# Performance work log

Measured on AMD Instinct MI355X. Metric: run time of the kernel, lower is better.

## Reference

```python
import jax, jax.numpy as jnp
import numpy as np

B, S, H = 32, 512, 768
NHEAD, DH = 8, 96          # 8 heads * 96 = 768
E = 4096                   # edges per sample
NC = 2
NEG = -1e9
EPS = 1e-5


def _p(k, shape, scale=0.02):
    return scale * jax.random.normal(k, shape, dtype=jnp.float32)


def setup_inputs() -> dict:
    key = jax.random.key(0)
    ks = jax.random.split(key, 24)
    z = lambda *s: jnp.zeros(s, jnp.float32)
    return {
        "diff_encoded": jax.random.normal(ks[0], (B, S, H), jnp.float32),
        "msg_encoded": jax.random.normal(ks[1], (B, S, H), jnp.float32),
        "msg_mask": jnp.ones((B, S), jnp.int32),
        "edge_index_diff": jax.random.randint(ks[2], (B, 2, E), 0, S),
        "edge_index_msg": jax.random.randint(ks[3], (B, 2, E), 0, S),
        # GATv2Conv(heads=1): lin_l (source/message), lin_r (target), att vector, output bias
        "gat_wl": _p(ks[4], (H, H)), "gat_bl": z(H),
        "gat_wr": _p(ks[5], (H, H)), "gat_br": z(H),
        "gat_att": _p(ks[6], (H,)), "gat_bias": z(H),
        # cross MultiheadAttention
        "wq": _p(ks[7], (H, H)), "bq": z(H),
        "wk": _p(ks[8], (H, H)), "bk": z(H),
        "wv": _p(ks[9], (H, H)), "bv": z(H),
        "wo": _p(ks[10], (H, H)), "bo": z(H),
        # LayerNorm + MLP head
        "ln_g": jnp.ones((H,), jnp.float32), "ln_b": z(H),
        "fc0_w": _p(ks[11], (H, 512)), "fc0_b": z(512),
        "fc1_w": _p(ks[12], (512, 128)), "fc1_b": z(128),
        "fc2_w": _p(ks[13], (128, NC)), "fc2_b": z(NC),
    }


def _gat_single(x, edges, wl, bl, wr, br, att, bias):
    # GATv2Conv, heads=1, add_self_loops=True. x: [N,H], edges: [2,E] (src, dst).
    N = x.shape[0]
    src, dst = edges[0], edges[1]
    valid = (src < N) & (dst < N)            # clip_edge_index, as a mask
    src = jnp.where(valid, src, 0)
    dst = jnp.where(valid, dst, 0)
    loop = jnp.arange(N, dtype=src.dtype)    # PyG adds self loops
    src_a = jnp.concatenate([src, loop])
    dst_a = jnp.concatenate([dst, loop])
    valid_a = jnp.concatenate([valid, jnp.ones((N,), bool)])
    xl = x @ wl + bl                          # source / message transform
    xr = x @ wr + br                          # target transform
    e = jax.nn.leaky_relu(xl[src_a] + xr[dst_a], 0.2) @ att   # [E+N]
    e = jnp.where(valid_a, e, NEG)
    emax = jax.ops.segment_max(e, dst_a, num_segments=N)
    p = jnp.exp(e - emax[dst_a]) * valid_a.astype(x.dtype)
    denom = jax.ops.segment_sum(p, dst_a, num_segments=N)
    alpha = p / denom[dst_a]
    out = jax.ops.segment_sum(alpha[:, None] * xl[src_a], dst_a, num_segments=N)
    return out + bias


_gat = jax.vmap(_gat_single, in_axes=(0, 0) + (None,) * 6)


def _layernorm(x, g, b):
    mu = jnp.mean(x, -1, keepdims=True)
    var = jnp.mean(jnp.square(x - mu), -1, keepdims=True)
    return (x - mu) * jax.lax.rsqrt(var + EPS) * g + b


def reference(diff_encoded, msg_encoded, msg_mask, edge_index_diff, edge_index_msg,
              gat_wl, gat_bl, gat_wr, gat_br, gat_att, gat_bias,
              wq, bq, wk, bk, wv, bv, wo, bo, ln_g, ln_b,
              fc0_w, fc0_b, fc1_w, fc1_b, fc2_w, fc2_b):
    diff_g = _gat(diff_encoded, edge_index_diff, gat_wl, gat_bl, gat_wr, gat_br, gat_att, gat_bias) + diff_encoded
    msg_g = _gat(msg_encoded, edge_index_msg, gat_wl, gat_bl, gat_wr, gat_br, gat_att, gat_bias) + msg_encoded
    # cross attention: query=diff_g, key/value=msg_g, key_padding_mask = (msg_mask == 0)
    q = (diff_g @ wq + bq).reshape(B, S, NHEAD, DH)
    k = (msg_g @ wk + bk).reshape(B, S, NHEAD, DH)
    v = (msg_g @ wv + bv).reshape(B, S, NHEAD, DH)
    scores = jnp.einsum("bqhd,bkhd->bhqk", q, k) / jnp.sqrt(jnp.float32(DH))
    scores = jnp.where((msg_mask == 0)[:, None, None, :], NEG, scores)
    attn = jax.nn.softmax(scores, axis=-1)
    ctx = jnp.einsum("bhqk,bkhd->bqhd", attn, v).reshape(B, S, H) @ wo + bo
    fused = _layernorm(ctx + diff_g, ln_g, ln_b)
    x = fused[:, 0, :]                                  # CLS token
    x = jax.nn.relu(x @ fc0_w + fc0_b)                  # dropout = identity (eval)
    x = jax.nn.relu(x @ fc1_w + fc1_b)
    return x @ fc2_w + fc2_b
```

## Files before the change

### kernel.cpp

```cpp
#include <hip/hip_runtime.h>
#include <hip/hip_bf16.h>
#include <math.h>

#define BB 32
#define SS 512
#define HH 768
#define NHEADC 8
#define DHC 96
#define EE 4096
#define NCC 2
#define CAPC 128
#define CAP2 32
#define GSL 36
#define NEGV -1000000000.0f
#define EPSV 1e-5f

#define PREP_CVT  12288
#define PREP_WT   2304
#define PREP_BIAS 3
#define PREP_CNT  512
#define PREP_TOT  (PREP_CVT + PREP_WT + PREP_BIAS + PREP_CNT)

typedef __hip_bfloat16 bf16;
typedef __bf16 bf16x8 __attribute__((ext_vector_type(8)));
typedef float f32x4 __attribute__((ext_vector_type(4)));

static __device__ inline unsigned short f2bf_u(float f) {
  __hip_bfloat16 h = __float2bfloat16(f);
  return *(unsigned short*)&h;
}
static __device__ inline float bfu(unsigned short u) {
  return __uint_as_float(((unsigned int)u) << 16);
}
static __device__ inline float bf2f(bf16 h) { return __bfloat162float(h); }

static __device__ inline void gload16(const void* g, void* l) {
  __builtin_amdgcn_global_load_lds(
      (const __attribute__((address_space(1))) void*)g,
      (__attribute__((address_space(3))) void*)l, 16, 0, 0);
}

__global__ __launch_bounds__(256) void k_prep(
    const float* __restrict__ msg_enc, bf16* __restrict__ Abf,
    const float* __restrict__ gat_wl, const float* __restrict__ gat_wr,
    const float* __restrict__ wk, const float* __restrict__ wv,
    bf16* __restrict__ wtA, bf16* __restrict__ wtB,
    const float* __restrict__ gat_bl, const float* __restrict__ gat_br,
    const float* __restrict__ bk, const float* __restrict__ bv,
    float* __restrict__ biasA, float* __restrict__ biasB,
    const int* __restrict__ e_diff,
    int* __restrict__ dcnt, int* __restrict__ dsrc)
{
  int blk = blockIdx.x, tid = threadIdx.x;
  if (blk < PREP_CVT) {
    int i = (blk * 256 + tid) * 4;
    float4 v = *(const float4*)(msg_enc + i);
    ushort4 o;
    o.x = f2bf_u(v.x); o.y = f2bf_u(v.y); o.z = f2bf_u(v.z); o.w = f2bf_u(v.w);
    *(ushort4*)((unsigned short*)Abf + i) = o;
    return;
  }
  blk -= PREP_CVT;
  if (blk < PREP_WT) {
    int z = blk / 576, rr = blk - z * 576;
    int bx = rr % 24, by = rr / 24;
    const float* w; bf16* o;
    switch (z) {
      case 0: w = gat_wl; o = wtA; break;
      case 1: w = gat_wr; o = wtA + (size_t)HH * HH; break;
      case 2: w = wk;     o = wtB; break;
      default: w = wv;    o = wtB + (size_t)HH * HH; break;
    }
    __shared__ float t[32][33];
    int n0 = bx * 32, k0 = by * 32;
    int x = tid & 31, y = tid >> 5;
    for (int yy = y; yy < 32; yy += 8)
      t[yy][x] = w[(size_t)(k0 + yy) * HH + n0 + x];
    __syncthreads();
    for (int yy = y; yy < 32; yy += 8)
      o[(size_t)(n0 + yy) * HH + k0 + x] = __float2bfloat16(t[x][yy]);
    return;
  }
  blk -= PREP_WT;
  if (blk < PREP_BIAS) {
    int t = blk * 256 + tid;
    if (t < HH) {
      biasA[t] = gat_bl[t]; biasA[HH + t] = gat_br[t];
      biasB[t] = bk[t];     biasB[HH + t] = bv[t];
    }
    return;
  }
  blk -= PREP_BIAS;
  {
    int i = blk * 256 + tid;
    if (i >= BB * EE) return;
    int b = i / EE, j = i - b * EE;
    int s2 = e_diff[b * 2 * EE + j], d2 = e_diff[b * 2 * EE + EE + j];
    if (s2 >= 0 && s2 < SS && d2 == 0) {
      int pos = atomicAdd(&dcnt[b], 1);
      if (pos < CAPC) dsrc[b * CAPC + pos] = s2;
    }
    if (j == 0) {
      int pos = atomicAdd(&dcnt[b], 1);
      if (pos < CAPC) dsrc[b * CAPC + pos] = 0;
    }
  }
}

__global__ __launch_bounds__(512) void k_bin(
    const int* __restrict__ e_msg, int* __restrict__ cnt,
    int* __restrict__ offs, int* __restrict__ binned)
{
  __shared__ int lc[SS];
  __shared__ int tmp[SS];
  int b = blockIdx.x, t = threadIdx.x;
  lc[t] = 0;
  __syncthreads();
  int ss[8], dd[8];
  #pragma unroll
  for (int r = 0; r < 8; ++r) {
    int j = r * 512 + t;
    ss[r] = e_msg[b * 2 * EE + j];
    dd[r] = e_msg[b * 2 * EE + EE + j];
    if (ss[r] >= 0 && ss[r] < SS && dd[r] >= 0 && dd[r] < SS)
      atomicAdd(&lc[dd[r]], 1);
    else
      dd[r] = -1;
  }
  __syncthreads();
  int x = lc[t];
  tmp[t] = x;
  __syncthreads();
  for (int off = 1; off < SS; off <<= 1) {
    int u = (t >= off) ? tmp[t - off] : 0;
    __syncthreads();
    tmp[t] += u;
    __syncthreads();
  }
  int ex = tmp[t] - x;
  cnt[b * SS + t] = x;
  offs[b * SS + t] = ex;
  __syncthreads();
  lc[t] = ex;
  __syncthreads();
  #pragma unroll
  for (int r = 0; r < 8; ++r) {
    if (dd[r] >= 0) {
      int pos = atomicAdd(&lc[dd[r]], 1);
      binned[(size_t)b * EE + pos] = ss[r];
    }
  }
}

template <typename OT>
__global__ __launch_bounds__(256) void k_gemm(
    const bf16* __restrict__ A, const bf16* __restrict__ Bt,
    const float* __restrict__ bias, OT* __restrict__ C0, OT* __restrict__ C1,
    int M, int K)
{
  __shared__ __align__(16) bf16 As0[128 * 32];
  __shared__ __align__(16) bf16 As1[128 * 32];
  __shared__ __align__(16) bf16 Bs0[128 * 32];
  __shared__ __align__(16) bf16 Bs1[128 * 32];
  const int tid = threadIdx.x;
  const int wv = tid >> 6, lane = tid & 63;
  const int bm = blockIdx.x * 128, bn = blockIdx.y * 128;
  const int wm = (wv & 1) * 64, wn = (wv >> 1) * 64;
  const int m16 = lane & 15, half = lane >> 4;
  f32x4 acc[4][4];
  #pragma unroll
  for (int i = 0; i < 4; ++i)
    #pragma unroll
    for (int j = 0; j < 4; ++j) acc[i][j] = (f32x4){0.f, 0.f, 0.f, 0.f};

  const int c0 = tid, c1 = tid + 256;
  const int r0 = c0 >> 2, o0 = (c0 & 3) * 8;
  const int r1 = c1 >> 2, o1 = (c1 & 3) * 8;
  const size_t aB0 = (size_t)(bm + r0) * K + o0;
  const size_t aB1 = (size_t)(bm + r1) * K + o1;
  const size_t bB0 = (size_t)(bn + r0) * K + o0;
  const size_t bB1 = (size_t)(bn + r1) * K + o1;

  for (int k0 = 0; k0 < K; k0 += 64) {
    __syncthreads();
    gload16(A + aB0 + k0, As0 + (size_t)c0 * 8);
    gload16(A + aB1 + k0, As0 + (size_t)c1 * 8);
    gload16(A + aB0 + k0 + 32, As1 + (size_t)c0 * 8);
    gload16(A + aB1 + k0 + 32, As1 + (size_t)c1 * 8);
    gload16(Bt + bB0 + k0, Bs0 + (size_t)c0 * 8);
    gload16(Bt + bB1 + k0, Bs0 + (size_t)c1 * 8);
    gload16(Bt + bB0 + k0 + 32, Bs1 + (size_t)c0 * 8);
    gload16(Bt + bB1 + k0 + 32, Bs1 + (size_t)c1 * 8);
    __syncthreads();
    #pragma unroll
    for (int ks = 0; ks < 2; ++ks) {
      const bf16* Ah = ks ? As1 : As0;
      const bf16* Bh = ks ? Bs1 : Bs0;
      bf16x8 af[4], bfv[4];
      #pragma unroll
      for (int t = 0; t < 4; ++t) {
        af[t]  = *(const bf16x8*)(Ah + (wm + t * 16 + m16) * 32 + half * 8);
        bfv[t] = *(const bf16x8*)(Bh + (wn + t * 16 + m16) * 32 + half * 8);
      }
      #pragma unroll
      for (int i = 0; i < 4; ++i)
        #pragma unroll
        for (int j = 0; j < 4; ++j)
          acc[i][j] = __builtin_amdgcn_mfma_f32_16x16x32_bf16(af[i], bfv[j], acc[i][j], 0, 0, 0);
    }
  }
  #pragma unroll
  for (int i = 0; i < 4; ++i) {
    #pragma unroll
    for (int j = 0; j < 4; ++j) {
      int col = bn + wn + j * 16 + m16;
      float bv = bias ? bias[col] : 0.f;
      OT* Cb = (col < HH) ? C0 : C1;
      int cc = (col < HH) ? col : col - HH;
      #pragma unroll
      for (int r = 0; r < 4; ++r) {
        int row = bm + wm + i * 16 + half * 4 + r;
        float v = acc[i][j][r] + bv;
        if constexpr (sizeof(OT) == 2)
          Cb[(size_t)row * HH + cc] = (OT)__float2bfloat16(v);
        else
          Cb[(size_t)row * HH + cc] = v;
      }
    }
  }
}

__global__ __launch_bounds__(512) void k_gemm256(
    const bf16* __restrict__ A, const bf16* __restrict__ Bt,
    const float* __restrict__ bias, bf16* __restrict__ C0, bf16* __restrict__ C1)
{
  constexpr int K = 768;
  constexpr int NT = K / 64;
  __shared__ __align__(16) bf16 Asm[3][256 * 64];
  __shared__ __align__(16) bf16 Bsm[3][128 * 64];

  const int tid = threadIdx.x;
  const int wv = tid >> 6, lane = tid & 63;
  const int m16 = lane & 15, half = lane >> 4;

  const int bid = blockIdx.x;
  const int swz = (bid & 7) * 96 + (bid >> 3);
  const int bm = (swz / 12) * 256;
  const int bn = (swz % 12) * 128;

  const int wm = (wv >> 1) * 64;
  const int wn = (wv & 1) * 64;

  size_t srcA[4], srcB[2];
  #pragma unroll
  for (int li = 0; li < 4; ++li) {
    int L = li * 512 + tid;
    int row = L >> 3;
    int g = (L & 7) ^ (row & 7);
    srcA[li] = (size_t)(bm + row) * K + g * 8;
  }
  #pragma unroll
  for (int li = 0; li < 2; ++li) {
    int L = li * 512 + tid;
    int row = L >> 3;
    int g = (L & 7) ^ (row & 7);
    srcB[li] = (size_t)(bn + row) * K + g * 8;
  }

  auto stage = [&](int t, bf16* ba, bf16* bb) {
    #pragma unroll
    for (int li = 0; li < 4; ++li)
      gload16(A + srcA[li] + (size_t)t * 64, ba + (size_t)(li * 512 + tid) * 8);
    #pragma unroll
    for (int li = 0; li < 2; ++li)
      gload16(Bt + srcB[li] + (size_t)t * 64, bb + (size_t)(li * 512 + tid) * 8);
  };

  f32x4 acc[4][4];
  #pragma unroll
  for (int i = 0; i < 4; ++i)
    #pragma unroll
    for (int j = 0; j < 4; ++j) acc[i][j] = (f32x4){0.f, 0.f, 0.f, 0.f};

  const int xr = m16 & 7;
  const int aoff0 = (wm + m16) * 64 + ((half ^ xr) * 8);
  const int aoff1 = (wm + m16) * 64 + (((4 + half) ^ xr) * 8);
  const int boff0 = (wn + m16) * 64 + ((half ^ xr) * 8);
  const int boff1 = (wn + m16) * 64 + (((4 + half) ^ xr) * 8);

  auto tile = [&](const bf16* __restrict__ Ab, const bf16* __restrict__ Bb) {
    bf16x8 b0[4], b1[4], a0[2], a1[2], a2[2], a3[2];
    #pragma unroll
    for (int j = 0; j < 4; ++j) b0[j] = *(const bf16x8*)(Bb + boff0 + j * 1024);
    #pragma unroll
    for (int i = 0; i < 2; ++i) a0[i] = *(const bf16x8*)(Ab + aoff0 + i * 1024);
    __builtin_amdgcn_s_setprio(1);
    #pragma unroll
    for (int i = 0; i < 2; ++i)
      #pragma unroll
      for (int j = 0; j < 4; ++j)
        acc[i][j] = __builtin_amdgcn_mfma_f32_16x16x32_bf16(a0[i], b0[j], acc[i][j], 0, 0, 0);
    __builtin_amdgcn_s_setprio(0);
    #pragma unroll
    for (int i = 0; i < 2; ++i) a1[i] = *(const bf16x8*)(Ab + aoff0 + (i + 2) * 1024);
    __builtin_amdgcn_s_setprio(1);
    #pragma unroll
    for (int i = 0; i < 2; ++i)
      #pragma unroll
      for (int j = 0; j < 4; ++j)
        acc[i + 2][j] = __builtin_amdgcn_mfma_f32_16x16x32_bf16(a1[i], b0[j], acc[i + 2][j], 0, 0, 0);
    __builtin_amdgcn_s_setprio(0);
    #pragma unroll
    for (int j = 0; j < 4; ++j) b1[j] = *(const bf16x8*)(Bb + boff1 + j * 1024);
    #pragma unroll
    for (int i = 0; i < 2; ++i) a2[i] = *(const bf16x8*)(Ab + aoff1 + i * 1024);
    __builtin_amdgcn_s_setprio(1);
    #pragma unroll
    for (int i = 0; i < 2; ++i)
      #pragma unroll
      for (int j = 0; j < 4; ++j)
        acc[i][j] = __builtin_amdgcn_mfma_f32_16x16x32_bf16(a2[i], b1[j], acc[i][j], 0, 0, 0);
    __builtin_amdgcn_s_setprio(0);
    #pragma unroll
    for (int i = 0; i < 2; ++i) a3[i] = *(const bf16x8*)(Ab + aoff1 + (i + 2) * 1024);
    __builtin_amdgcn_s_setprio(1);
    #pragma unroll
    for (int i = 0; i < 2; ++i)
      #pragma unroll
      for (int j = 0; j < 4; ++j)
        acc[i + 2][j] = __builtin_amdgcn_mfma_f32_16x16x32_bf16(a3[i], b1[j], acc[i + 2][j], 0, 0, 0);
    __builtin_amdgcn_s_setprio(0);
  };

  auto step = [&](int kt, int cur, int nxt) {
    if (kt == NT - 1) asm volatile("s_waitcnt vmcnt(0)" ::: "memory");
    else              asm volatile("s_waitcnt vmcnt(6)" ::: "memory");
    __builtin_amdgcn_s_barrier();
    __builtin_amdgcn_sched_barrier(0);
    if (kt + 2 < NT) stage(kt + 2, Asm[nxt], Bsm[nxt]);
    tile(Asm[cur], Bsm[cur]);
  };

  stage(0, Asm[0], Bsm[0]);
  stage(1, Asm[1], Bsm[1]);
  for (int kt3 = 0; kt3 < NT; kt3 += 3) {
    step(kt3 + 0, 0, 2);
    step(kt3 + 1, 1, 0);
    step(kt3 + 2, 2, 1);
  }

  #pragma unroll
  for (int i = 0; i < 4; ++i) {
    #pragma unroll
    for (int j = 0; j < 4; ++j) {
      int col = bn + wn + j * 16 + m16;
      float bv = bias[col];
      bf16* Cb = (col < HH) ? C0 : C1;
      int cc = (col < HH) ? col : col - HH;
      #pragma unroll
      for (int r = 0; r < 4; ++r) {
        int row = bm + wm + i * 16 + half * 4 + r;
        Cb[(size_t)row * HH + cc] = (bf16)__float2bfloat16(acc[i][j][r] + bv);
      }
    }
  }
}

__global__ __launch_bounds__(256) void k_gat_fused(
    const int* __restrict__ binned, const int* __restrict__ offs,
    const int* __restrict__ cnt, const bf16* __restrict__ xl,
    const bf16* __restrict__ xrb, const float* __restrict__ att,
    const float* __restrict__ gbias, const bf16* __restrict__ resid,
    bf16* __restrict__ out)
{
  int bid = blockIdx.x;
  int xcd = bid & 7, idx = bid >> 3;
  int b = xcd * 4 + (idx >> 7);
  int d = (idx & 127) * 4 + (threadIdx.x >> 6);
  int lane = threadIdx.x & 63;
  int base = offs[b * SS + d], n = cnt[b * SS + d];
  const int* bin = binned + (size_t)b * EE + base;
  float av[12];
  {
    const float4* a4 = (const float4*)att;
    #pragma unroll
    for (int r = 0; r < 3; ++r) {
      float4 t = a4[lane + 64 * r];
      av[4*r] = t.x; av[4*r+1] = t.y; av[4*r+2] = t.z; av[4*r+3] = t.w;
    }
  }
  float xr[12];
  {
    const ushort4* p = (const ushort4*)(xrb + ((size_t)b * SS + d) * HH);
    #pragma unroll
    for (int r = 0; r < 3; ++r) {
      ushort4 v = p[lane + 64 * r];
      xr[4*r] = bfu(v.x); xr[4*r+1] = bfu(v.y); xr[4*r+2] = bfu(v.z); xr[4*r+3] = bfu(v.w);
    }
  }
  float m = -3.0e38f, l = 0.f;
  float acc[12] = {};
  int nn = n + 1;
  ushort4 pre[3];
  {
    const ushort4* p = (const ushort4*)(xl + ((size_t)b * SS + d) * HH);
    pre[0] = p[lane]; pre[1] = p[lane + 64]; pre[2] = p[lane + 128];
  }
  for (int j = 0; j < nn; ++j) {
    ushort4 cur0 = pre[0], cur1 = pre[1], cur2 = pre[2];
    if (j + 1 < nn) {
      int sn = bin[j];
      const ushort4* p = (const ushort4*)(xl + ((size_t)b * SS + sn) * HH);
      pre[0] = p[lane]; pre[1] = p[lane + 64]; pre[2] = p[lane + 128];
    }
    float xs[12];
    xs[0] = bfu(cur0.x); xs[1] = bfu(cur0.y); xs[2]  = bfu(cur0.z); xs[3]  = bfu(cur0.w);
    xs[4] = bfu(cur1.x); xs[5] = bfu(cur1.y); xs[6]  = bfu(cur1.z); xs[7]  = bfu(cur1.w);
    xs[8] = bfu(cur2.x); xs[9] = bfu(cur2.y); xs[10] = bfu(cur2.z); xs[11] = bfu(cur2.w);
    float e = 0.f;
    #pragma unroll
    for (int k = 0; k < 12; ++k) {
      float t = xs[k] + xr[k];
      t = t > 0.f ? t : 0.2f * t;
      e += t * av[k];
    }
    #pragma unroll
    for (int off = 32; off > 0; off >>= 1) e += __shfl_xor(e, off);
    float mn = fmaxf(m, e);
    float so = __expf(m - mn);
    float w  = __expf(e - mn);
    l = l * so + w;
    #pragma unroll
    for (int k = 0; k < 12; ++k) acc[k] = acc[k] * so + w * xs[k];
    m = mn;
  }
  float inv = 1.f / l;
  size_t o = ((size_t)b * SS + d) * HH;
  const float4* gb4 = (const float4*)gbias;
  const ushort4* rs4 = (const ushort4*)(resid + o);
  ushort4* out4 = (ushort4*)(out + o);
  #pragma unroll
  for (int r = 0; r < 3; ++r) {
    int c = lane + 64 * r;
    float4 gg = gb4[c];
    ushort4 rr = rs4[c];
    ushort4 ov;
    ov.x = f2bf_u(acc[4*r+0] * inv + gg.x + bfu(rr.x));
    ov.y = f2bf_u(acc[4*r+1] * inv + gg.y + bfu(rr.y));
    ov.z = f2bf_u(acc[4*r+2] * inv + gg.z + bfu(rr.z));
    ov.w = f2bf_u(acc[4*r+3] * inv + gg.w + bfu(rr.w));
    out4[c] = ov;
  }
}

__global__ __launch_bounds__(192) void k_gather_diff(
    const int* __restrict__ dcnt, const int* __restrict__ dsrc,
    const float* __restrict__ diff_enc, bf16* __restrict__ G)
{
  int b = blockIdx.y, jj = blockIdx.x;
  int n = min(dcnt[b], CAP2);
  int t = threadIdx.x;
  size_t orow = ((size_t)b * GSL + jj) * HH;
  ushort4 o = {0, 0, 0, 0};
  if (jj < n || jj == CAP2) {
    int s = (jj == CAP2) ? 0 : dsrc[b * CAPC + jj];
    float4 v = ((const float4*)(diff_enc + ((size_t)b * SS + s) * HH))[t];
    o.x = f2bf_u(v.x); o.y = f2bf_u(v.y); o.z = f2bf_u(v.z); o.w = f2bf_u(v.w);
  }
  *(ushort4*)((unsigned short*)G + orow + t * 4) = o;
}

__global__ __launch_bounds__(256) void k_diff_gat0(
    const int* __restrict__ dcnt, const float* __restrict__ GDl,
    const float* __restrict__ GDr, const float* __restrict__ att,
    const float* __restrict__ gbias, const float* __restrict__ diff_enc,
    float* __restrict__ dg0)
{
  int b = blockIdx.x;
  int n = min(dcnt[b], CAP2);
  __shared__ float ee[CAP2];
  __shared__ float al[CAP2];
  __shared__ float xr0s[HH];
  int wave = threadIdx.x >> 6, lane = threadIdx.x & 63;
  for (int h = threadIdx.x; h < HH; h += 256)
    xr0s[h] = GDr[((size_t)b * GSL + CAP2) * HH + h];
  __syncthreads();
  for (int jj = wave; jj < n; jj += 4) {
    const float* px = GDl + ((size_t)b * GSL + jj) * HH;
    float part = 0.f;
    #pragma unroll
    for (int r = 0; r < HH / 64; ++r) {
      int h = lane + 64 * r;
      float t = px[h] + xr0s[h];
      t = t > 0.f ? t : 0.2f * t;
      part += t * att[h];
    }
    #pragma unroll
    for (int off = 32; off > 0; off >>= 1) part += __shfl_xor(part, off);
    if (lane == 0) ee[jj] = part;
  }
  __syncthreads();
  if (threadIdx.x == 0) {
    float m = -3.0e38f;
    for (int i = 0; i < n; ++i) m = fmaxf(m, ee[i]);
    float ssum = 0.f;
    for (int i = 0; i < n; ++i) ssum += expf(ee[i] - m);
    float inv = 1.f / ssum;
    for (int i = 0; i < n; ++i) al[i] = expf(ee[i] - m) * inv;
  }
  __syncthreads();
  for (int h = threadIdx.x; h < HH; h += 256) {
    float acc = 0.f;
    for (int i = 0; i < n; ++i) acc += al[i] * GDl[((size_t)b * GSL + i) * HH + h];
    dg0[b * HH + h] = acc + gbias[h] + diff_enc[(size_t)b * SS * HH + h];
  }
}

__global__ __launch_bounds__(256) void k_colmat(
    const float* __restrict__ in, const float* __restrict__ w,
    const float* __restrict__ bias, const float* __restrict__ extra,
    float* __restrict__ outp, int Kd, int Nd, long in_stride, int relu)
{
  int b = blockIdx.y, n0 = blockIdx.x * 64;
  int tid = threadIdx.x, wv = tid >> 6, lane = tid & 63;
  __shared__ float xs[HH];
  __shared__ float red[4][64];
  const float* src = in + (size_t)b * in_stride;
  for (int k = tid; k < Kd; k += 256) xs[k] = src[k];
  __syncthreads();
  int h = n0 + lane;
  int kpw = Kd >> 2;
  int kb = wv * kpw;
  float acc = 0.f;
  for (int k = 0; k < kpw; k += 8) {
    #pragma unroll
    for (int u = 0; u < 8; ++u) {
      int kk = kb + k + u;
      acc += xs[kk] * w[(size_t)kk * Nd + h];
    }
  }
  red[wv][lane] = acc;
  __syncthreads();
  if (tid < 64) {
    float s = red[0][tid] + red[1][tid] + red[2][tid] + red[3][tid] + bias[n0 + tid];
    if (extra) s += extra[(size_t)b * Nd + n0 + tid];
    if (relu) s = fmaxf(s, 0.f);
    outp[(size_t)b * Nd + n0 + tid] = s;
  }
}

__global__ __launch_bounds__(256) void k_lnfc0(
    const float* __restrict__ fpre, const float* __restrict__ g,
    const float* __restrict__ bta,
    const float* __restrict__ fc0w, const float* __restrict__ fc0b,
    float* __restrict__ a0g)
{
  int b = blockIdx.y, n0 = blockIdx.x * 64;
  int tid = threadIdx.x, wv = tid >> 6, lane = tid & 63;
  __shared__ float xs[HH];
  __shared__ float red[4][64];
  __shared__ float rs[4], rq[4];
  float v0 = fpre[b * HH + tid];
  float v1 = fpre[b * HH + tid + 256];
  float v2 = fpre[b * HH + tid + 512];
  float sum = v0 + v1 + v2;
  float sq = v0 * v0 + v1 * v1 + v2 * v2;
  #pragma unroll
  for (int off = 32; off > 0; off >>= 1) { sum += __shfl_xor(sum, off); sq += __shfl_xor(sq, off); }
  if (lane == 0) { rs[wv] = sum; rq[wv] = sq; }
  __syncthreads();
  sum = rs[0] + rs[1] + rs[2] + rs[3];
  sq = rq[0] + rq[1] + rq[2] + rq[3];
  float mu = sum / HH;
  float var = sq / HH - mu * mu;
  float scl = rsqrtf(var + EPSV);
  xs[tid]       = (v0 - mu) * scl * g[tid]       + bta[tid];
  xs[tid + 256] = (v1 - mu) * scl * g[tid + 256] + bta[tid + 256];
  xs[tid + 512] = (v2 - mu) * scl * g[tid + 512] + bta[tid + 512];
  __syncthreads();
  int h = n0 + lane;
  int kb = wv * 192;
  float acc = 0.f;
  for (int k = 0; k < 192; k += 8) {
    #pragma unroll
    for (int u = 0; u < 8; ++u) {
      int kk = kb + k + u;
      acc += xs[kk] * fc0w[(size_t)kk * 512 + h];
    }
  }
  red[wv][lane] = acc;
  __syncthreads();
  if (tid < 64) {
    float s = red[0][tid] + red[1][tid] + red[2][tid] + red[3][tid] + fc0b[n0 + tid];
    a0g[(size_t)b * 512 + n0 + tid] = fmaxf(s, 0.f);
  }
}

__global__ __launch_bounds__(256) void k_fc12(
    const float* __restrict__ a0g, const float* __restrict__ fc1w,
    const float* __restrict__ fc1b, const float* __restrict__ fc2w,
    const float* __restrict__ fc2b, float* __restrict__ out)
{
  int b = blockIdx.x, tid = threadIdx.x;
  __shared__ float a0s[512];
  __shared__ float a1s[128];
  __shared__ float r1[2][128];
  for (int k = tid; k < 512; k += 256) a0s[k] = a0g[b * 512 + k];
  __syncthreads();
  int o = tid & 127, hf = tid >> 7;
  int kb = hf * 256;
  float acc = 0.f;
  for (int k = 0; k < 256; k += 8) {
    #pragma unroll
    for (int u = 0; u < 8; ++u) {
      int kk = kb + k + u;
      acc += a0s[kk] * fc1w[(size_t)kk * 128 + o];
    }
  }
  r1[hf][o] = acc;
  __syncthreads();
  if (tid < 128) a1s[tid] = fmaxf(r1[0][tid] + r1[1][tid] + fc1b[tid], 0.f);
  __syncthreads();
  if (tid < 128) {
    int oo = tid >> 6, l = tid & 63;
    float p = a1s[l] * fc2w[l * 2 + oo] + a1s[l + 64] * fc2w[(l + 64) * 2 + oo];
    #pragma unroll
    for (int off = 32; off > 0; off >>= 1) p += __shfl_xor(p, off);
    if (l == 0) out[b * NCC + oo] = p + fc2b[oo];
  }
}

__global__ __launch_bounds__(512) void k_attn(
    const float* __restrict__ dg0, const float* __restrict__ wq,
    const float* __restrict__ bq, const bf16* __restrict__ kb,
    const bf16* __restrict__ vb, const int* __restrict__ mask,
    float* __restrict__ ctx)
{
  int b = blockIdx.x / NHEADC, hd = blockIdx.x % NHEADC;
  __shared__ float xg[HH];
  __shared__ float qs[DHC];
  __shared__ float sc[SS];
  __shared__ float redm[8];
  __shared__ float reds[8];
  __shared__ float pr4[4][DHC];
  int tid = threadIdx.x;
  for (int k = tid; k < HH; k += 512) xg[k] = dg0[b * HH + k];
  __syncthreads();
  if (tid < 384) {
    int d = tid >> 2, q = tid & 3;
    const float* wcol = wq + (size_t)(hd * DHC + d);
    float p = 0.f;
    int k0 = q * 192;
    for (int k = 0; k < 192; k += 8) {
      #pragma unroll
      for (int u = 0; u < 8; ++u)
        p += xg[k0 + k + u] * wcol[(size_t)(k0 + k + u) * HH];
    }
    p += __shfl_xor(p, 1);
    p += __shfl_xor(p, 2);
    if (q == 0) qs[d] = p + bq[hd * DHC + d];
  }
  __syncthreads();
  const float scale = 0.10206207261596575f;
  {
    int s = tid;
    const int4* pk4 = (const int4*)(kb + ((size_t)b * SS + s) * HH + hd * DHC);
    float acc = 0.f;
    #pragma unroll
    for (int c = 0; c < 12; ++c) {
      int4 raw = pk4[c];
      const unsigned short* u = (const unsigned short*)&raw;
      #pragma unroll
      for (int j = 0; j < 8; ++j) acc += qs[c * 8 + j] * bfu(u[j]);
    }
    sc[s] = (mask[b * SS + s] != 0) ? acc * scale : NEGV;
  }
  __syncthreads();
  int wave = tid >> 6, lane = tid & 63;
  float m = sc[tid];
  #pragma unroll
  for (int off = 32; off > 0; off >>= 1) m = fmaxf(m, __shfl_xor(m, off));
  if (lane == 0) redm[wave] = m;
  __syncthreads();
  m = redm[0];
  #pragma unroll
  for (int i = 1; i < 8; ++i) m = fmaxf(m, redm[i]);
  float p0 = expf(sc[tid] - m);
  float ssum = p0;
  #pragma unroll
  for (int off = 32; off > 0; off >>= 1) ssum += __shfl_xor(ssum, off);
  if (lane == 0) reds[wave] = ssum;
  __syncthreads();
  ssum = reds[0] + reds[1] + reds[2] + reds[3] + reds[4] + reds[5] + reds[6] + reds[7];
  float inv = 1.f / ssum;
  sc[tid] = p0 * inv;
  __syncthreads();
  {
    int hs = tid >> 7, d = tid & 127;
    if (d < DHC) {
      const bf16* pv = vb + ((size_t)b * SS + hs * 128) * HH + hd * DHC + d;
      float acc = 0.f;
      for (int s = 0; s < 128; s += 8) {
        #pragma unroll
        for (int u = 0; u < 8; ++u)
          acc += sc[hs * 128 + s + u] * bf2f(pv[(size_t)(s + u) * HH]);
      }
      pr4[hs][d] = acc;
    }
  }
  __syncthreads();
  if (tid < DHC)
    ctx[b * HH + hd * DHC + tid] = pr4[0][tid] + pr4[1][tid] + pr4[2][tid] + pr4[3][tid];
}

extern "C" void kernel_launch(void* const* d_in, const int* in_sizes, int n_in,
                              void* d_out, int out_size, void* d_ws, size_t ws_size,
                              hipStream_t stream) {
  const float* diff_enc = (const float*)d_in[0];
  const float* msg_enc  = (const float*)d_in[1];
  const int*   msg_mask = (const int*)d_in[2];
  const int*   e_diff   = (const int*)d_in[3];
  const int*   e_msg    = (const int*)d_in[4];
  const float* gat_wl   = (const float*)d_in[5];
  const float* gat_bl   = (const float*)d_in[6];
  const float* gat_wr   = (const float*)d_in[7];
  const float* gat_br   = (const float*)d_in[8];
  const float* gat_att  = (const float*)d_in[9];
  const float* gat_bias = (const float*)d_in[10];
  const float* wq = (const float*)d_in[11];
  const float* bq = (const float*)d_in[12];
  const float* wk = (const float*)d_in[13];
  const float* bk = (const float*)d_in[14];
  const float* wv = (const float*)d_in[15];
  const float* bv = (const float*)d_in[16];
  const float* wo = (const float*)d_in[17];
  const float* bo = (const float*)d_in[18];
  const float* ln_g = (const float*)d_in[19];
  const float* ln_b = (const float*)d_in[20];
  const float* fc0w = (const float*)d_in[21];
  const float* fc0b = (const float*)d_in[22];
  const float* fc1w = (const float*)d_in[23];
  const float* fc1b = (const float*)d_in[24];
  const float* fc2w = (const float*)d_in[25];
  const float* fc2b = (const float*)d_in[26];
  float* out = (float*)d_out;

  char* ws = (char*)d_ws;
  size_t off = 0;
  auto alloc = [&](size_t bytes) -> void* {
    void* p = (void*)(ws + off);
    off += (bytes + 255) & ~(size_t)255;
    return p;
  };
  bf16* Abf    = (bf16*)alloc((size_t)BB * SS * HH * 2);
  bf16* xl     = (bf16*)alloc((size_t)BB * SS * HH * 2);
  bf16* xrb    = (bf16*)alloc((size_t)BB * SS * HH * 2);
  bf16* kbuf   = (bf16*)alloc((size_t)BB * SS * HH * 2);
  bf16* vbuf   = (bf16*)alloc((size_t)BB * SS * HH * 2);
  bf16* mg     = (bf16*)alloc((size_t)BB * SS * HH * 2);
  bf16* wtA    = (bf16*)alloc((size_t)2 * HH * HH * 2);
  bf16* wtB    = (bf16*)alloc((size_t)2 * HH * HH * 2);
  float* biasA = (float*)alloc((size_t)2 * HH * 4);
  float* biasB = (float*)alloc((size_t)2 * HH * 4);
  int*   cnt   = (int*)alloc((size_t)BB * SS * 4);
  int*   offs  = (int*)alloc((size_t)BB * SS * 4);
  int*   binned= (int*)alloc((size_t)BB * EE * 4);
  bf16*  G     = (bf16*)alloc((size_t)BB * GSL * HH * 2);
  float* GDl   = (float*)alloc((size_t)BB * GSL * HH * 4);
  float* GDr   = (float*)alloc((size_t)BB * GSL * HH * 4);
  int*   dcnt  = (int*)alloc((size_t)BB * 4);
  int*   dsrc  = (int*)alloc((size_t)BB * CAPC * 4);
  float* dg0   = (float*)alloc((size_t)BB * HH * 4);
  float* ctx   = (float*)alloc((size_t)BB * HH * 4);
  float* fpre  = (float*)alloc((size_t)BB * HH * 4);
  float* a0g   = (float*)alloc((size_t)BB * 512 * 4);

  hipMemsetAsync(dcnt, 0, (size_t)BB * 4, stream);

  k_prep<<<PREP_TOT, 256, 0, stream>>>(msg_enc, Abf, gat_wl, gat_wr, wk, wv,
                                       wtA, wtB, gat_bl, gat_br, bk, bv,
                                       biasA, biasB, e_diff, dcnt, dsrc);
  k_bin<<<BB, 512, 0, stream>>>(e_msg, cnt, offs, binned);

  k_gemm256<<<768, 512, 0, stream>>>(Abf, wtA, biasA, xl, xrb);
  k_gat_fused<<<(BB * SS) / 4, 256, 0, stream>>>(binned, offs, cnt, xl, xrb,
                                                 gat_att, gat_bias, Abf, mg);
  k_gemm256<<<768, 512, 0, stream>>>(mg, wtB, biasB, kbuf, vbuf);
  {
    dim3 gBlk(256);
    dim3 gg(GSL, BB);
    k_gather_diff<<<gg, 192, 0, stream>>>(dcnt, dsrc, diff_enc, G);
    dim3 gGridD((BB * GSL) / 128, (2 * HH) / 128);
    k_gemm<float><<<gGridD, gBlk, 0, stream>>>(G, wtA, biasA, GDl, GDr, BB * GSL, HH);
  }
  k_diff_gat0<<<BB, 256, 0, stream>>>(dcnt, GDl, GDr, gat_att, gat_bias, diff_enc, dg0);
  k_attn<<<BB * NHEADC, 512, 0, stream>>>(dg0, wq, bq, kbuf, vbuf, msg_mask, ctx);
  {
    dim3 g(HH / 64, BB);
    k_colmat<<<g, 256, 0, stream>>>(ctx, wo, bo, dg0, fpre, HH, HH, HH, 0);
  }
  {
    dim3 g(512 / 64, BB);
    k_lnfc0<<<g, 256, 0, stream>>>(fpre, ln_g, ln_b, fc0w, fc0b, a0g);
  }
  k_fc12<<<BB, 256, 0, stream>>>(a0g, fc1w, fc1b, fc2w, fc2b, out);
}
```

Baseline: 424.6 us.

## Fold edge binning into prep and merge diff-gather GEMM into main GEMM

Merges the msg-edge binning kernel and the diff-edge collection into the prep kernel, with the diff collection now done through shared memory instead of global atomics. This removes the memset and a separate launch. The gathered diff rows (GSL raised to 40 so the row count divides into 256-row tiles) are appended after the msg activations, so one larger k_gemm256 launch computes both xl/xr and GDl/GDr. Its XCD swizzle is generalised to arbitrary tile counts. The intent is fewer launches and no small, poorly occupied separate GEMM, at the cost of slightly more padded rows and a heavier prep block.

```diff
diff --git a/kernel.cpp b/kernel.cpp
--- a/kernel.cpp
+++ b/kernel.cpp
@@ -11,15 +11,15 @@
 #define NCC 2
 #define CAPC 128
 #define CAP2 32
-#define GSL 36
+#define GSL 40
 #define NEGV -1000000000.0f
 #define EPSV 1e-5f
 
-#define PREP_CVT  12288
+#define PREP_CVT  6144
 #define PREP_WT   2304
-#define PREP_BIAS 3
-#define PREP_CNT  512
-#define PREP_TOT  (PREP_CVT + PREP_WT + PREP_BIAS + PREP_CNT)
+#define PREP_BIAS 2
+#define PREP_BIN  BB
+#define PREP_TOT  (PREP_CVT + PREP_WT + PREP_BIAS + PREP_BIN)
 
 typedef __hip_bfloat16 bf16;
 typedef __bf16 bf16x8 __attribute__((ext_vector_type(8)));
@@ -40,7 +40,7 @@
       (__attribute__((address_space(3))) void*)l, 16, 0, 0);
 }
 
-__global__ __launch_bounds__(256) void k_prep(
+__global__ __launch_bounds__(512) void k_prep(
     const float* __restrict__ msg_enc, bf16* __restrict__ Abf,
     const float* __restrict__ gat_wl, const float* __restrict__ gat_wr,
     const float* __restrict__ wk, const float* __restrict__ wv,
@@ -48,12 +48,13 @@
     const float* __restrict__ gat_bl, const float* __restrict__ gat_br,
     const float* __restrict__ bk, const float* __restrict__ bv,
     float* __restrict__ biasA, float* __restrict__ biasB,
-    const int* __restrict__ e_diff,
+    const int* __restrict__ e_msg, const int* __restrict__ e_diff,
+    int* __restrict__ cnt, int* __restrict__ offs, int* __restrict__ binned,
     int* __restrict__ dcnt, int* __restrict__ dsrc)
 {
   int blk = blockIdx.x, tid = threadIdx.x;
   if (blk < PREP_CVT) {
-    int i = (blk * 256 + tid) * 4;
+    int i = (blk * 512 + tid) * 4;
     float4 v = *(const float4*)(msg_enc + i);
     ushort4 o;
     o.x = f2bf_u(v.x); o.y = f2bf_u(v.y); o.z = f2bf_u(v.z); o.w = f2bf_u(v.w);
@@ -74,16 +75,16 @@
     __shared__ float t[32][33];
     int n0 = bx * 32, k0 = by * 32;
     int x = tid & 31, y = tid >> 5;
-    for (int yy = y; yy < 32; yy += 8)
+    for (int yy = y; yy < 32; yy += 16)
       t[yy][x] = w[(size_t)(k0 + yy) * HH + n0 + x];
     __syncthreads();
-    for (int yy = y; yy < 32; yy += 8)
+    for (int yy = y; yy < 32; yy += 16)
       o[(size_t)(n0 + yy) * HH + k0 + x] = __float2bfloat16(t[x][yy]);
     return;
   }
   blk -= PREP_WT;
   if (blk < PREP_BIAS) {
-    int t = blk * 256 + tid;
+    int t = blk * 512 + tid;
     if (t < HH) {
       biasA[t] = gat_bl[t]; biasA[HH + t] = gat_br[t];
       biasB[t] = bk[t];     biasB[HH + t] = bv[t];
@@ -92,139 +93,63 @@
   }
   blk -= PREP_BIAS;
   {
-    int i = blk * 256 + tid;
-    if (i >= BB * EE) return;
-    int b = i / EE, j = i - b * EE;
-    int s2 = e_diff[b * 2 * EE + j], d2 = e_diff[b * 2 * EE + EE + j];
-    if (s2 >= 0 && s2 < SS && d2 == 0) {
-      int pos = atomicAdd(&dcnt[b], 1);
-      if (pos < CAPC) dsrc[b * CAPC + pos] = s2;
-    }
-    if (j == 0) {
-      int pos = atomicAdd(&dcnt[b], 1);
-      if (pos < CAPC) dsrc[b * CAPC + pos] = 0;
-    }
-  }
-}
-
-__global__ __launch_bounds__(512) void k_bin(
-    const int* __restrict__ e_msg, int* __restrict__ cnt,
-    int* __restrict__ offs, int* __restrict__ binned)
-{
-  __shared__ int lc[SS];
-  __shared__ int tmp[SS];
-  int b = blockIdx.x, t = threadIdx.x;
-  lc[t] = 0;
-  __syncthreads();
-  int ss[8], dd[8];
-  #pragma unroll
-  for (int r = 0; r < 8; ++r) {
-    int j = r * 512 + t;
-    ss[r] = e_msg[b * 2 * EE + j];
-    dd[r] = e_msg[b * 2 * EE + EE + j];
-    if (ss[r] >= 0 && ss[r] < SS && dd[r] >= 0 && dd[r] < SS)
-      atomicAdd(&lc[dd[r]], 1);
-    else
-      dd[r] = -1;
-  }
-  __syncthreads();
-  int x = lc[t];
-  tmp[t] = x;
-  __syncthreads();
-  for (int off = 1; off < SS; off <<= 1) {
-    int u = (t >= off) ? tmp[t - off] : 0;
+    __shared__ int lc[SS];
+    __shared__ int tmp[SS];
+    __shared__ int dls[CAPC];
+    __shared__ int dn;
+    int b = blk, t = tid;
+    lc[t] = 0;
+    if (t == 0) dn = 0;
     __syncthreads();
-    tmp[t] += u;
+    int se[8], de[8];
+    #pragma unroll
+    for (int r = 0; r < 8; ++r) {
+      int j = r * 512 + t;
+      se[r] = e_msg[b * 2 * EE + j];
+      de[r] = e_msg[b * 2 * EE + EE + j];
+      if (se[r] >= 0 && se[r] < SS && de[r] >= 0 && de[r] < SS)
+        atomicAdd(&lc[de[r]], 1);
+      else
+        de[r] = -1;
+    }
+    #pragma unroll
+    for (int r = 0; r < 8; ++r) {
+      int j = r * 512 + t;
+      int s2 = e_diff[b * 2 * EE + j], d2 = e_diff[b * 2 * EE + EE + j];
+      if (s2 >= 0 && s2 < SS && d2 == 0) {
+        int p = atomicAdd(&dn, 1);
+        if (p < CAPC) dls[p] = s2;
+      }
+    }
+    if (t == 0) {
+      int p = atomicAdd(&dn, 1);
+      if (p < CAPC) dls[p] = 0;
+    }
     __syncthreads();
-  }
-  int ex = tmp[t] - x;
-  cnt[b * SS + t] = x;
-  offs[b * SS + t] = ex;
-  __syncthreads();
-  lc[t] = ex;
-  __syncthreads();
-  #pragma unroll
-  for (int r = 0; r < 8; ++r) {
-    if (dd[r] >= 0) {
-      int pos = atomicAdd(&lc[dd[r]], 1);
-      binned[(size_t)b * EE + pos] = ss[r];
-    }
-  }
-}
-
-template <typename OT>
-__global__ __launch_bounds__(256) void k_gemm(
-    const bf16* __restrict__ A, const bf16* __restrict__ Bt,
-    const float* __restrict__ bias, OT* __restrict__ C0, OT* __restrict__ C1,
-    int M, int K)
-{
-  __shared__ __align__(16) bf16 As0[128 * 32];
-  __shared__ __align__(16) bf16 As1[128 * 32];
-  __shared__ __align__(16) bf16 Bs0[128 * 32];
-  __shared__ __align__(16) bf16 Bs1[128 * 32];
-  const int tid = threadIdx.x;
-  const int wv = tid >> 6, lane = tid & 63;
-  const int bm = blockIdx.x * 128, bn = blockIdx.y * 128;
-  const int wm = (wv & 1) * 64, wn = (wv >> 1) * 64;
-  const int m16 = lane & 15, half = lane >> 4;
-  f32x4 acc[4][4];
-  #pragma unroll
-  for (int i = 0; i < 4; ++i)
-    #pragma unroll
-    for (int j = 0; j < 4; ++j) acc[i][j] = (f32x4){0.f, 0.f, 0.f, 0.f};
-
-  const int c0 = tid, c1 = tid + 256;
-  const int r0 = c0 >> 2, o0 = (c0 & 3) * 8;
-  const int r1 = c1 >> 2, o1 = (c1 & 3) * 8;
-  const size_t aB0 = (size_t)(bm + r0) * K + o0;
-  const size_t aB1 = (size_t)(bm + r1) * K + o1;
-  const size_t bB0 = (size_t)(bn + r0) * K + o0;
-  const size_t bB1 = (size_t)(bn + r1) * K + o1;
-
-  for (int k0 = 0; k0 < K; k0 += 64) {
+    int x = lc[t];
+    tmp[t] = x;
     __syncthreads();
-    gload16(A + aB0 + k0, As0 + (size_t)c0 * 8);
-    gload16(A + aB1 + k0, As0 + (size_t)c1 * 8);
-    gload16(A + aB0 + k0 + 32, As1 + (size_t)c0 * 8);
-    gload16(A + aB1 + k0 + 32, As1 + (size_t)c1 * 8);
-    gload16(Bt + bB0 + k0, Bs0 + (size_t)c0 * 8);
-    gload16(Bt + bB1 + k0, Bs0 + (size_t)c1 * 8);
-    gload16(Bt + bB0 + k0 + 32, Bs1 + (size_t)c0 * 8);
-    gload16(Bt + bB1 + k0 + 32, Bs1 + (size_t)c1 * 8);
+    for (int off = 1; off < SS; off <<= 1) {
+      int u = (t >= off) ? tmp[t - off] : 0;
+      __syncthreads();
+      tmp[t] += u;
+      __syncthreads();
+    }
+    int ex = tmp[t] - x;
+    cnt[b * SS + t] = x;
+    offs[b * SS + t] = ex;
+    int dnl = dn;
+    if (t == 0) dcnt[b] = dnl;
+    if (dnl > CAPC) dnl = CAPC;
+    for (int i2 = t; i2 < dnl; i2 += 512) dsrc[b * CAPC + i2] = dls[i2];
     __syncthreads();
-    #pragma unroll
-    for (int ks = 0; ks < 2; ++ks) {
-      const bf16* Ah = ks ? As1 : As0;
-      const bf16* Bh = ks ? Bs1 : Bs0;
-      bf16x8 af[4], bfv[4];
-      #pragma unroll
-      for (int t = 0; t < 4; ++t) {
-        af[t]  = *(const bf16x8*)(Ah + (wm + t * 16 + m16) * 32 + half * 8);
-        bfv[t] = *(const bf16x8*)(Bh + (wn + t * 16 + m16) * 32 + half * 8);
-      }
-      #pragma unroll
-      for (int i = 0; i < 4; ++i)
-        #pragma unroll
-        for (int j = 0; j < 4; ++j)
-          acc[i][j] = __builtin_amdgcn_mfma_f32_16x16x32_bf16(af[i], bfv[j], acc[i][j], 0, 0, 0);
-    }
-  }
-  #pragma unroll
-  for (int i = 0; i < 4; ++i) {
-    #pragma unroll
-    for (int j = 0; j < 4; ++j) {
-      int col = bn + wn + j * 16 + m16;
-      float bv = bias ? bias[col] : 0.f;
-      OT* Cb = (col < HH) ? C0 : C1;
-      int cc = (col < HH) ? col : col - HH;
-      #pragma unroll
-      for (int r = 0; r < 4; ++r) {
-        int row = bm + wm + i * 16 + half * 4 + r;
-        float v = acc[i][j][r] + bv;
-        if constexpr (sizeof(OT) == 2)
-          Cb[(size_t)row * HH + cc] = (OT)__float2bfloat16(v);
-        else
-          Cb[(size_t)row * HH + cc] = v;
+    lc[t] = ex;
+    __syncthreads();
+    #pragma unroll
+    for (int r = 0; r < 8; ++r) {
+      if (de[r] >= 0) {
+        int pos = atomicAdd(&lc[de[r]], 1);
+        binned[(size_t)b * EE + pos] = se[r];
       }
     }
   }
@@ -232,10 +157,13 @@
 
 __global__ __launch_bounds__(512) void k_gemm256(
     const bf16* __restrict__ A, const bf16* __restrict__ Bt,
-    const float* __restrict__ bias, bf16* __restrict__ C0, bf16* __restrict__ C1)
+    const float* __restrict__ bias,
+    bf16* __restrict__ C0, bf16* __restrict__ C1,
+    float* __restrict__ D0, float* __restrict__ D1, int nmt)
 {
   constexpr int K = 768;
   constexpr int NT = K / 64;
+  constexpr int M0 = BB * SS;
   __shared__ __align__(16) bf16 Asm[3][256 * 64];
   __shared__ __align__(16) bf16 Bsm[3][128 * 64];
 
@@ -244,7 +172,10 @@
   const int m16 = lane & 15, half = lane >> 4;
 
   const int bid = blockIdx.x;
-  const int swz = (bid & 7) * 96 + (bid >> 3);
+  const int nwg = nmt * 12;
+  const int qq = nwg >> 3, rm = nwg & 7;
+  const int xcd = bid & 7, iblk = bid >> 3;
+  const int swz = (xcd < rm ? xcd * (qq + 1) : rm * (qq + 1) + (xcd - rm) * qq) + iblk;
   const int bm = (swz / 12) * 256;
   const int bn = (swz % 12) * 128;
 
@@ -349,18 +280,28 @@
     step(kt3 + 2, 2, 1);
   }
 
+  const bool isD = (bm >= M0);
   #pragma unroll
   for (int i = 0; i < 4; ++i) {
     #pragma unroll
     for (int j = 0; j < 4; ++j) {
       int col = bn + wn + j * 16 + m16;
       float bv = bias[col];
-      bf16* Cb = (col < HH) ? C0 : C1;
       int cc = (col < HH) ? col : col - HH;
-      #pragma unroll
-      for (int r = 0; r < 4; ++r) {
-        int row = bm + wm + i * 16 + half * 4 + r;
-        Cb[(size_t)row * HH + cc] = (bf16)__float2bfloat16(acc[i][j][r] + bv);
+      if (!isD) {
+        bf16* Cb = (col < HH) ? C0 : C1;
+        #pragma unroll
+        for (int rj = 0; rj < 4; ++rj) {
+          int row = bm + wm + i * 16 + half * 4 + rj;
+          Cb[(size_t)row * HH + cc] = (bf16)__float2bfloat16(acc[i][j][rj] + bv);
+        }
+      } else {
+        float* Db = (col < HH) ? D0 : D1;
+        #pragma unroll
+        for (int rj = 0; rj < 4; ++rj) {
+          int row = bm + wm + i * 16 + half * 4 + rj - M0;
+          Db[(size_t)row * HH + cc] = acc[i][j][rj] + bv;
+        }
       }
     }
   }
@@ -752,7 +693,8 @@
     off += (bytes + 255) & ~(size_t)255;
     return p;
   };
-  bf16* Abf    = (bf16*)alloc((size_t)BB * SS * HH * 2);
+  bf16* Abf    = (bf16*)alloc((size_t)(BB * SS + BB * GSL) * HH * 2);
+  bf16* G      = Abf + (size_t)BB * SS * HH;
   bf16* xl     = (bf16*)alloc((size_t)BB * SS * HH * 2);
   bf16* xrb    = (bf16*)alloc((size_t)BB * SS * HH * 2);
   bf16* kbuf   = (bf16*)alloc((size_t)BB * SS * HH * 2);
@@ -765,7 +707,6 @@
   int*   cnt   = (int*)alloc((size_t)BB * SS * 4);
   int*   offs  = (int*)alloc((size_t)BB * SS * 4);
   int*   binned= (int*)alloc((size_t)BB * EE * 4);
-  bf16*  G     = (bf16*)alloc((size_t)BB * GSL * HH * 2);
   float* GDl   = (float*)alloc((size_t)BB * GSL * HH * 4);
   float* GDr   = (float*)alloc((size_t)BB * GSL * HH * 4);
   int*   dcnt  = (int*)alloc((size_t)BB * 4);
@@ -775,24 +716,19 @@
   float* fpre  = (float*)alloc((size_t)BB * HH * 4);
   float* a0g   = (float*)alloc((size_t)BB * 512 * 4);
 
-  hipMemsetAsync(dcnt, 0, (size_t)BB * 4, stream);
-
-  k_prep<<<PREP_TOT, 256, 0, stream>>>(msg_enc, Abf, gat_wl, gat_wr, wk, wv,
+  k_prep<<<PREP_TOT, 512, 0, stream>>>(msg_enc, Abf, gat_wl, gat_wr, wk, wv,
                                        wtA, wtB, gat_bl, gat_br, bk, bv,
-                                       biasA, biasB, e_diff, dcnt, dsrc);
-  k_bin<<<BB, 512, 0, stream>>>(e_msg, cnt, offs, binned);
-
-  k_gemm256<<<768, 512, 0, stream>>>(Abf, wtA, biasA, xl, xrb);
+                                       biasA, biasB, e_msg, e_diff,
+                                       cnt, offs, binned, dcnt, dsrc);
+  {
+    dim3 gg(GSL, BB);
+    k_gather_diff<<<gg, 192, 0, stream>>>(dcnt, dsrc, diff_enc, G);
+  }
+  const int NMT1 = (BB * SS + BB * GSL) / 256;
+  k_gemm256<<<NMT1 * 12, 512, 0, stream>>>(Abf, wtA, biasA, xl, xrb, GDl, GDr, NMT1);
   k_gat_fused<<<(BB * SS) / 4, 256, 0, stream>>>(binned, offs, cnt, xl, xrb,
                                                  gat_att, gat_bias, Abf, mg);
-  k_gemm256<<<768, 512, 0, stream>>>(mg, wtB, biasB, kbuf, vbuf);
-  {
-    dim3 gBlk(256);
-    dim3 gg(GSL, BB);
-    k_gather_diff<<<gg, 192, 0, stream>>>(dcnt, dsrc, diff_enc, G);
-    dim3 gGridD((BB * GSL) / 128, (2 * HH) / 128);
-    k_gemm<float><<<gGridD, gBlk, 0, stream>>>(G, wtA, biasA, GDl, GDr, BB * GSL, HH);
-  }
+  k_gemm256<<<768, 512, 0, stream>>>(mg, wtB, biasB, kbuf, vbuf, nullptr, nullptr, 64);
   k_diff_gat0<<<BB, 256, 0, stream>>>(dcnt, GDl, GDr, gat_att, gat_bias, diff_enc, dg0);
   k_attn<<<BB * NHEADC, 512, 0, stream>>>(dg0, wq, bq, kbuf, vbuf, msg_mask, ctx);
   {
```

Result: faster. 414.8 us (-2.3%).
